# Kernel tuning notes

Hardware: AMD Instinct MI355X
Metric: run time of the kernel (lower is better)

## Reference

```python
import jax, jax.numpy as jnp
import numpy as np

N_HEAD = 16
MASK_PENALTY = 10000.0


def setup_inputs() -> dict:
    key = jax.random.key(0)
    k1, k2, k3 = jax.random.split(key, 3)
    B, S, D = 2, 2048, 1024
    x = jax.random.normal(k1, (B, S, D), dtype=jnp.float32)
    w_attn = jax.random.normal(k2, (D, 3 * D), dtype=jnp.float32) * 0.02
    b_attn = jnp.zeros((3 * D,), dtype=jnp.float32)
    w_proj = jax.random.normal(k3, (D, D), dtype=jnp.float32) * 0.02
    b_proj = jnp.zeros((D,), dtype=jnp.float32)
    return {"x": x, "w_attn": w_attn, "b_attn": b_attn, "w_proj": w_proj, "b_proj": b_proj}


def _split_heads(t, n_head):
    B, S, D = t.shape
    return t.reshape(B, S, n_head, D // n_head).transpose(0, 2, 1, 3)  # [B,H,S,dh]


def reference(x, w_attn, b_attn, w_proj, b_proj):
    B, S, D = x.shape
    qkv = x @ w_attn + b_attn  # fused QKV conv1d: [B,S,3D]
    q, k, v = jnp.split(qkv, 3, axis=2)
    q = _split_heads(q, N_HEAD)
    k = _split_heads(k, N_HEAD)
    v = _split_heads(v, N_HEAD)
    dh = D // N_HEAD
    w = jnp.einsum("bhqd,bhkd->bhqk", q, k) / jnp.sqrt(jnp.asarray(dh, dtype=q.dtype))
    # GPT-2 additive causal mask: w*b - 10000*(1-b)
    i = jnp.arange(S)[:, None]
    j = jnp.arange(S)[None, :]
    b = (i >= j).astype(w.dtype)  # nd == ns here
    w = w * b - MASK_PENALTY * (1.0 - b)
    w = jax.nn.softmax(w, axis=-1)
    a = jnp.einsum("bhqk,bhkd->bhqd", w, v)  # [B,H,S,dh]
    a = a.transpose(0, 2, 1, 3).reshape(B, S, D)  # merge heads
    return a @ w_proj + b_proj
```

## Files before the change

kernel.cpp:

```cpp
#include <hip/hip_runtime.h>
#include <hip/hip_bf16.h>


typedef short short8 __attribute__((ext_vector_type(8)));
typedef float f32x4 __attribute__((ext_vector_type(4)));

__device__ __forceinline__ unsigned short f2b(float f) {
    unsigned int x;
    __builtin_memcpy(&x, &f, 4);
    unsigned int r = x + 0x7FFF + ((x >> 16) & 1);
    return (unsigned short)(r >> 16);
}

__device__ __forceinline__ unsigned int pk2(float a, float b) {
    __hip_bfloat162 h = __float22bfloat162_rn(make_float2(a, b));
    unsigned int u;
    __builtin_memcpy(&u, &h, 4);
    return u;
}

__device__ __forceinline__ void load_lds16(const unsigned short* g, unsigned short* l) {
    __builtin_amdgcn_global_load_lds(
        (const __attribute__((address_space(1))) unsigned int*)g,
        (__attribute__((address_space(3))) unsigned int*)l, 16, 0, 0);
}

__global__ __launch_bounds__(256) void prep(const float* __restrict__ x, unsigned int* __restrict__ xb,
                                            const float* __restrict__ wA, unsigned short* __restrict__ wtA,
                                            const float* __restrict__ wP, unsigned short* __restrict__ wtP) {
    const int bx = blockIdx.x, tid = threadIdx.x;
    if (bx < 1024) {
#pragma unroll
        for (int j = 0; j < 4; j++) {
            int i = (bx * 1024 + j * 256 + tid) * 4;
            float4 f = *(const float4*)(x + i);
            uint2 p;
            p.x = pk2(f.x, f.y);
            p.y = pk2(f.z, f.w);
            *(uint2*)(xb + i / 2) = p;
        }
        return;
    }
    __shared__ unsigned short T[64][72];
    const float* in;
    unsigned short* out;
    int R, C, r0, c0;
    if (bx < 1792) { int t = bx - 1024; c0 = (t % 48) * 64; r0 = (t / 48) * 64; in = wA; out = wtA; R = 1024; C = 3072; }
    else           { int t = bx - 1792; c0 = (t % 16) * 64; r0 = (t / 16) * 64; in = wP; out = wtP; R = 1024; C = 1024; }
    const int ty = tid >> 4, tx = tid & 15;
#pragma unroll
    for (int i = 0; i < 4; i++) {
        int row = ty + i * 16;
        float4 f = *(const float4*)(in + (size_t)(r0 + row) * C + c0 + tx * 4);
        T[tx * 4 + 0][row] = f2b(f.x);
        T[tx * 4 + 1][row] = f2b(f.y);
        T[tx * 4 + 2][row] = f2b(f.z);
        T[tx * 4 + 3][row] = f2b(f.w);
    }
    __syncthreads();
    const int c = tid >> 2, rq = tid & 3;
    const uint4* s = (const uint4*)&T[c][rq * 16];
    uint4 a = s[0], b = s[1];
    unsigned short* dst = out + (size_t)(c0 + c) * R + r0 + rq * 16;
    *(uint4*)dst = a;
    *(uint4*)(dst + 8) = b;
}

__global__ __launch_bounds__(256) void qkv_gemm(const unsigned short* __restrict__ X,
                                                const unsigned short* __restrict__ WT,
                                                const float* __restrict__ bias,
                                                unsigned short* __restrict__ Qo,
                                                unsigned short* __restrict__ Ko,
                                                unsigned short* __restrict__ Vt) {
    __shared__ __align__(16) unsigned short SM[16384];
    unsigned short* As = SM;
    unsigned short* Bs = SM + 8192;
    const int tid = threadIdx.x;
    const int w = tid >> 6, l = tid & 63, l15 = l & 15, quad = l >> 4;
    const int wr = w >> 1, wc = w & 1;
    const int m0 = blockIdx.y * 128, n0 = blockIdx.x * 128;

    const int sr = w * 16 + (l >> 2);
    const int gch = (l & 3) ^ ((l >> 3) & 3);
    const unsigned short* Asrc = X + (size_t)(m0 + sr) * 1024 + gch * 8;
    const unsigned short* Bsrc = WT + (size_t)(n0 + sr) * 1024 + gch * 8;
    const int rswz = (l15 >> 1) & 3;

    f32x4 acc[4][4];
#pragma unroll
    for (int mt = 0; mt < 4; mt++)
#pragma unroll
        for (int nt = 0; nt < 4; nt++) acc[mt][nt] = (f32x4){0.f, 0.f, 0.f, 0.f};

    load_lds16(Asrc, &As[tid * 8]);
    load_lds16(Asrc + 65536, &As[2048 + tid * 8]);
    load_lds16(Bsrc, &Bs[tid * 8]);
    load_lds16(Bsrc + 65536, &Bs[2048 + tid * 8]);

    for (int k0 = 0; k0 < 1024; k0 += 32) {
        const int c = (k0 >> 5) & 1;
        __syncthreads();
        if (k0 + 32 < 1024) {
            const int pc = 1 - c;
            load_lds16(Asrc + k0 + 32, &As[pc * 4096 + tid * 8]);
            load_lds16(Asrc + 65536 + k0 + 32, &As[pc * 4096 + 2048 + tid * 8]);
            load_lds16(Bsrc + k0 + 32, &Bs[pc * 4096 + tid * 8]);
            load_lds16(Bsrc + 65536 + k0 + 32, &Bs[pc * 4096 + 2048 + tid * 8]);
        }

        short8 af[4], bfr[4];
#pragma unroll
        for (int mt = 0; mt < 4; mt++)
            af[mt] = *(const short8*)&As[c * 4096 + (wr * 64 + mt * 16 + l15) * 32 + ((quad ^ rswz) * 8)];
#pragma unroll
        for (int nt = 0; nt < 4; nt++)
            bfr[nt] = *(const short8*)&Bs[c * 4096 + (wc * 64 + nt * 16 + l15) * 32 + ((quad ^ rswz) * 8)];
#pragma unroll
        for (int mt = 0; mt < 4; mt++)
#pragma unroll
            for (int nt = 0; nt < 4; nt++)
                acc[mt][nt] = __builtin_amdgcn_mfma_f32_16x16x32_bf16(af[mt], bfr[nt], acc[mt][nt], 0, 0, 0);
    }

    const int which = n0 >> 10;
    const int c0 = n0 & 1023;
    float bv[4];
#pragma unroll
    for (int nt = 0; nt < 4; nt++) bv[nt] = bias[n0 + wc * 64 + nt * 16 + l15];

    if (which < 2) {
        const float scale = (which == 1) ? 0.125f : 1.0f;
        unsigned short* dst = (which == 0) ? Qo : Ko;
#pragma unroll
        for (int mt = 0; mt < 4; mt++)
#pragma unroll
            for (int nt = 0; nt < 4; nt++)
#pragma unroll
                for (int r = 0; r < 4; r++) {
                    int mg = m0 + wr * 64 + mt * 16 + quad * 4 + r;
                    int cg = c0 + wc * 64 + nt * 16 + l15;
                    float v = (acc[mt][nt][r] + bv[nt]) * scale;
                    int h = cg >> 6, d = cg & 63;
                    dst[(((size_t)(mg >> 11) * 16 + h) * 2048 + (mg & 2047)) * 64 + d] = f2b(v);
                }
    } else {
        const int b = m0 >> 11, sbase = m0 & 2047, h0 = c0 >> 6;
#pragma unroll
        for (int p = 0; p < 2; p++) {
            __syncthreads();
            if (wc == p) {
#pragma unroll
                for (int mt = 0; mt < 4; mt++)
#pragma unroll
                    for (int nt = 0; nt < 4; nt++)
#pragma unroll
                        for (int r = 0; r < 4; r++) {
                            float v = acc[mt][nt][r] + bv[nt];
                            int d = nt * 16 + l15;
                            int mloc = wr * 64 + mt * 16 + quad * 4 + r;
                            SM[d * 128 + (((mloc >> 4) ^ (d & 7)) << 4) + (mloc & 15)] = f2b(v);
                        }
            }
            __syncthreads();
            const int d = tid >> 2, q4 = tid & 3;
            size_t gb = ((size_t)((b * 16 + h0 + p) * 64 + d)) * 2048 + sbase + q4 * 32;
#pragma unroll
            for (int half = 0; half < 2; half++) {
                int mc = q4 * 2 + half;
                const uint4* s = (const uint4*)&SM[d * 128 + ((mc ^ (d & 7)) << 4)];
                *(uint4*)(Vt + gb + half * 16) = s[0];
                *(uint4*)(Vt + gb + half * 16 + 8) = s[1];
            }
        }
    }
}

__global__ __launch_bounds__(256) void attn_k(const unsigned short* __restrict__ Q,
                                              const unsigned short* __restrict__ K,
                                              const unsigned short* __restrict__ Vt,
                                              unsigned short* __restrict__ Om) {
    __shared__ __align__(16) unsigned short SM[20480];
    unsigned short* Ks0 = SM;
    unsigned short* Vts0 = SM + 8192;
    unsigned short* QP = SM + 16384;

    const int tid = threadIdx.x;
    const int w = tid >> 6, l = tid & 63, l15 = l & 15, quad = l >> 4;
    const int wq = w >> 1, ws = w & 1;
    const int bid = blockIdx.x;
    const int pi = bid >> 5;
    const int hb = bid & 31;
    const unsigned short* Qb = Q + (size_t)hb * 131072;
    const unsigned short* Kb = K + (size_t)hb * 131072;
    const unsigned short* Vb = Vt + (size_t)hb * 131072;

    const int sr = w * 8 + (l >> 3);
    const int gch = (l & 7) ^ (l >> 3);
    const int swz7 = l15 & 7;
    const int b = hb >> 4, h = hb & 15;

    short8 ones;
#pragma unroll
    for (int j = 0; j < 8; j++) ones[j] = (short)0x3F80;

    for (int half = 0; half < 2; half++) {
        const int qt = half ? pi : (31 - pi);
        const int q0 = qt * 64;

        if (half) __syncthreads();

        load_lds16(Qb + (q0 + sr) * 64 + gch * 8, &QP[tid * 8]);
        load_lds16(Qb + (q0 + 32 + sr) * 64 + gch * 8, &QP[2048 + tid * 8]);
        load_lds16(Kb + sr * 64 + gch * 8, &Ks0[tid * 8]);
        load_lds16(Kb + (32 + sr) * 64 + gch * 8, &Ks0[2048 + tid * 8]);
        load_lds16(Vb + sr * 2048 + gch * 8, &Vts0[tid * 8]);
        load_lds16(Vb + (32 + sr) * 2048 + gch * 8, &Vts0[2048 + tid * 8]);
        __syncthreads();

        short8 qf[2][2];
#pragma unroll
        for (int qnt = 0; qnt < 2; qnt++)
#pragma unroll
            for (int ks = 0; ks < 2; ks++)
                qf[qnt][ks] = *(const short8*)&QP[(wq * 32 + qnt * 16 + l15) * 64 + (((ks * 4 + quad) ^ swz7) << 3)];

        f32x4 o[2][4], lacc[2];
#pragma unroll
        for (int pmt = 0; pmt < 2; pmt++) {
            lacc[pmt] = (f32x4){0.f, 0.f, 0.f, 0.f};
#pragma unroll
            for (int dnt = 0; dnt < 4; dnt++) o[pmt][dnt] = (f32x4){0.f, 0.f, 0.f, 0.f};
        }

        for (int kt = 0; kt <= qt; kt++) {
            const int c = kt & 1;
            const unsigned short* Ksc = Ks0 + c * 4096;
            const unsigned short* Vtsc = Vts0 + c * 4096;
            __syncthreads();
            if (kt < qt) {
                const int kn = (kt + 1) * 64, pc = 1 - c;
                load_lds16(Kb + (kn + sr) * 64 + gch * 8, &Ks0[pc * 4096 + tid * 8]);
                load_lds16(Kb + (kn + 32 + sr) * 64 + gch * 8, &Ks0[pc * 4096 + 2048 + tid * 8]);
                load_lds16(Vb + sr * 2048 + kn + gch * 8, &Vts0[pc * 4096 + tid * 8]);
                load_lds16(Vb + (32 + sr) * 2048 + kn + gch * 8, &Vts0[pc * 4096 + 2048 + tid * 8]);
            }

            f32x4 sa[2][2];
#pragma unroll
            for (int smt = 0; smt < 2; smt++)
#pragma unroll
                for (int qnt = 0; qnt < 2; qnt++) sa[smt][qnt] = (f32x4){0.f, 0.f, 0.f, 0.f};
#pragma unroll
            for (int ks = 0; ks < 2; ks++) {
                short8 kf[2];
#pragma unroll
                for (int smt = 0; smt < 2; smt++)
                    kf[smt] = *(const short8*)&Ksc[(ws * 32 + smt * 16 + l15) * 64 + (((ks * 4 + quad) ^ swz7) << 3)];
#pragma unroll
                for (int smt = 0; smt < 2; smt++)
#pragma unroll
                    for (int qnt = 0; qnt < 2; qnt++)
                        sa[smt][qnt] = __builtin_amdgcn_mfma_f32_16x16x32_bf16(kf[smt], qf[qnt][ks], sa[smt][qnt], 0, 0, 0);
            }

            float pv[2][2][4];
            if (kt == qt) {
#pragma unroll
                for (int smt = 0; smt < 2; smt++)
#pragma unroll
                    for (int qnt = 0; qnt < 2; qnt++)
#pragma unroll
                        for (int r = 0; r < 4; r++) {
                            int cg = kt * 64 + ws * 32 + smt * 16 + quad * 4 + r;
                            int rg = q0 + wq * 32 + qnt * 16 + l15;
                            pv[smt][qnt][r] = (cg <= rg) ? __expf(sa[smt][qnt][r]) : 0.f;
                        }
            } else {
#pragma unroll
                for (int smt = 0; smt < 2; smt++)
#pragma unroll
                    for (int qnt = 0; qnt < 2; qnt++)
#pragma unroll
                        for (int r = 0; r < 4; r++)
                            pv[smt][qnt][r] = __expf(sa[smt][qnt][r]);
            }

#pragma unroll
            for (int smt = 0; smt < 2; smt++)
#pragma unroll
                for (int qnt = 0; qnt < 2; qnt++) {
                    int q = wq * 32 + qnt * 16 + l15;
                    int sb = ws * 32 + smt * 16 + quad * 4;
                    int ch = (sb >> 3) ^ (q & 7);
                    int a16 = q * 64 + (ch << 3) + (sb & 7);
                    uint2 u;
                    u.x = pk2(pv[smt][qnt][0], pv[smt][qnt][1]);
                    u.y = pk2(pv[smt][qnt][2], pv[smt][qnt][3]);
                    *(uint2*)&QP[a16] = u;
                }
            asm volatile("s_waitcnt lgkmcnt(0)" ::: "memory");

            short8 pf[2];
#pragma unroll
            for (int pmt = 0; pmt < 2; pmt++) {
                pf[pmt] = *(const short8*)&QP[(wq * 32 + pmt * 16 + l15) * 64 + (((ws * 4 + quad) ^ swz7) << 3)];
                lacc[pmt] = __builtin_amdgcn_mfma_f32_16x16x32_bf16(pf[pmt], ones, lacc[pmt], 0, 0, 0);
            }
#pragma unroll
            for (int dnt = 0; dnt < 4; dnt++) {
                short8 vf = *(const short8*)&Vtsc[(dnt * 16 + l15) * 64 + (((ws * 4 + quad) ^ swz7) << 3)];
#pragma unroll
                for (int pmt = 0; pmt < 2; pmt++)
                    o[pmt][dnt] = __builtin_amdgcn_mfma_f32_16x16x32_bf16(pf[pmt], vf, o[pmt][dnt], 0, 0, 0);
            }
        }

        __syncthreads();
        float* red = (float*)SM;
        float* myp = red + (wq * 64 + l) * 41;
        if (ws == 1) {
#pragma unroll
            for (int pmt = 0; pmt < 2; pmt++) {
#pragma unroll
                for (int dnt = 0; dnt < 4; dnt++)
#pragma unroll
                    for (int r = 0; r < 4; r++) myp[pmt * 16 + dnt * 4 + r] = o[pmt][dnt][r];
#pragma unroll
                for (int r = 0; r < 4; r++) myp[32 + pmt * 4 + r] = lacc[pmt][r];
            }
        }
        __syncthreads();
        if (ws == 0) {
            float inv[2][4];
#pragma unroll
            for (int pmt = 0; pmt < 2; pmt++)
#pragma unroll
                for (int r = 0; r < 4; r++)
                    inv[pmt][r] = 1.0f / (lacc[pmt][r] + myp[32 + pmt * 4 + r]);
#pragma unroll
            for (int pmt = 0; pmt < 2; pmt++)
#pragma unroll
                for (int dnt = 0; dnt < 4; dnt++)
#pragma unroll
                    for (int r = 0; r < 4; r++) {
                        float val = (o[pmt][dnt][r] + myp[pmt * 16 + dnt * 4 + r]) * inv[pmt][r];
                        int sg = q0 + wq * 32 + pmt * 16 + quad * 4 + r;
                        int col = h * 64 + dnt * 16 + l15;
                        Om[((size_t)(b * 2048 + sg)) * 1024 + col] = f2b(val);
                    }
        }
    }
}

__global__ __launch_bounds__(256) void proj_gemm(const unsigned short* __restrict__ A,
                                                 const unsigned short* __restrict__ WT,
                                                 const float* __restrict__ bias,
                                                 float* __restrict__ out) {
    __shared__ __align__(16) unsigned short As[2][4096];
    __shared__ __align__(16) unsigned short Bs[2][2048];
    const int tid = threadIdx.x;
    const int w = tid >> 6, l = tid & 63, l15 = l & 15, quad = l >> 4;
    const int wr = w >> 1, wc = w & 1;
    const int m0 = blockIdx.y * 128, n0 = blockIdx.x * 64;

    const int sr = w * 16 + (l >> 2);
    const int gch = (l & 3) ^ ((l >> 3) & 3);
    const unsigned short* Asrc = A + (size_t)(m0 + sr) * 1024 + gch * 8;
    const unsigned short* Bsrc = WT + (size_t)(n0 + sr) * 1024 + gch * 8;
    const int rswz = (l15 >> 1) & 3;

    f32x4 acc[4][2];
#pragma unroll
    for (int mt = 0; mt < 4; mt++)
#pragma unroll
        for (int nt = 0; nt < 2; nt++) acc[mt][nt] = (f32x4){0.f, 0.f, 0.f, 0.f};

    load_lds16(Asrc, &As[0][tid * 8]);
    load_lds16(Asrc + 65536, &As[0][2048 + tid * 8]);
    load_lds16(Bsrc, &Bs[0][tid * 8]);

    for (int k0 = 0; k0 < 1024; k0 += 32) {
        const int c = (k0 >> 5) & 1;
        __syncthreads();
        if (k0 + 32 < 1024) {
            const int pc = 1 - c;
            load_lds16(Asrc + k0 + 32, &As[pc][tid * 8]);
            load_lds16(Asrc + 65536 + k0 + 32, &As[pc][2048 + tid * 8]);
            load_lds16(Bsrc + k0 + 32, &Bs[pc][tid * 8]);
        }

        short8 af[4], bfr[2];
#pragma unroll
        for (int mt = 0; mt < 4; mt++)
            af[mt] = *(const short8*)&As[c][(wr * 64 + mt * 16 + l15) * 32 + ((quad ^ rswz) * 8)];
#pragma unroll
        for (int nt = 0; nt < 2; nt++)
            bfr[nt] = *(const short8*)&Bs[c][(wc * 32 + nt * 16 + l15) * 32 + ((quad ^ rswz) * 8)];
#pragma unroll
        for (int mt = 0; mt < 4; mt++)
#pragma unroll
            for (int nt = 0; nt < 2; nt++)
                acc[mt][nt] = __builtin_amdgcn_mfma_f32_16x16x32_bf16(af[mt], bfr[nt], acc[mt][nt], 0, 0, 0);
    }

#pragma unroll
    for (int mt = 0; mt < 4; mt++)
#pragma unroll
        for (int nt = 0; nt < 2; nt++)
#pragma unroll
            for (int r = 0; r < 4; r++) {
                int mg = m0 + wr * 64 + mt * 16 + quad * 4 + r;
                int ng = n0 + wc * 32 + nt * 16 + l15;
                out[(size_t)mg * 1024 + ng] = acc[mt][nt][r] + bias[ng];
            }
}

extern "C" void kernel_launch(void* const* d_in, const int* in_sizes, int n_in,
                              void* d_out, int out_size, void* d_ws, size_t ws_size,
                              hipStream_t stream) {
    (void)in_sizes; (void)n_in; (void)out_size; (void)ws_size;
    const float* x      = (const float*)d_in[0];
    const float* w_attn = (const float*)d_in[1];
    const float* b_attn = (const float*)d_in[2];
    const float* w_proj = (const float*)d_in[3];
    const float* b_proj = (const float*)d_in[4];
    float* out = (float*)d_out;
    unsigned short* ws = (unsigned short*)d_ws;

    unsigned short* wtA  = ws;
    unsigned short* wtP  = wtA + 3145728;
    unsigned short* Qw   = wtP + 1048576;
    unsigned short* Kw   = Qw + 4194304;
    unsigned short* Vtw  = Kw + 4194304;
    unsigned short* XbOm = Vtw + 4194304;

    prep<<<2048, 256, 0, stream>>>(x, (unsigned int*)XbOm, w_attn, wtA, w_proj, wtP);
    qkv_gemm<<<dim3(24, 32), 256, 0, stream>>>(XbOm, wtA, b_attn, Qw, Kw, Vtw);
    attn_k<<<512, 256, 0, stream>>>(Qw, Kw, Vtw, XbOm);
    proj_gemm<<<dim3(16, 32), 256, 0, stream>>>(XbOm, wtP, b_proj, out);
}
```

Baseline: 176.5 us.

## Triple-buffer LDS pipelines with one barrier per step; split attention blocks per query tile

In all three GEMM-like kernels, the double-buffered LDS loop with a full __syncthreads becomes a three-stage ring. Each step issues the next tile's global-to-LDS loads, then runs s_waitcnt vmcnt(N) plus s_barrier, so only the older tile must land and one load group stays in flight. The attention kernel no longer pairs a long and a short causal query tile per block; it launches 1024 blocks with one query tile each and relies on the scheduler to balance the uneven work. LDS use per block grows, which may lower occupancy, and the last iterations issue redundant dummy loads.

```diff
diff --git a/kernel.cpp b/kernel.cpp
--- a/kernel.cpp
+++ b/kernel.cpp
@@ -4,6 +4,10 @@
 
 typedef short short8 __attribute__((ext_vector_type(8)));
 typedef float f32x4 __attribute__((ext_vector_type(4)));
+
+#define WAITB4 asm volatile("s_waitcnt vmcnt(4)\n\ts_barrier" ::: "memory")
+#define WAITB3 asm volatile("s_waitcnt vmcnt(3)\n\ts_barrier" ::: "memory")
+#define DRAIN0 asm volatile("s_waitcnt vmcnt(0)" ::: "memory")
 
 __device__ __forceinline__ unsigned short f2b(float f) {
     unsigned int x;
@@ -72,9 +76,9 @@
                                                 unsigned short* __restrict__ Qo,
                                                 unsigned short* __restrict__ Ko,
                                                 unsigned short* __restrict__ Vt) {
-    __shared__ __align__(16) unsigned short SM[16384];
+    __shared__ __align__(16) unsigned short SM[24576];
     unsigned short* As = SM;
-    unsigned short* Bs = SM + 8192;
+    unsigned short* Bs = SM + 12288;
     const int tid = threadIdx.x;
     const int w = tid >> 6, l = tid & 63, l15 = l & 15, quad = l >> 4;
     const int wr = w >> 1, wc = w & 1;
@@ -97,16 +101,15 @@
     load_lds16(Bsrc, &Bs[tid * 8]);
     load_lds16(Bsrc + 65536, &Bs[2048 + tid * 8]);
 
-    for (int k0 = 0; k0 < 1024; k0 += 32) {
-        const int c = (k0 >> 5) & 1;
-        __syncthreads();
-        if (k0 + 32 < 1024) {
-            const int pc = 1 - c;
-            load_lds16(Asrc + k0 + 32, &As[pc * 4096 + tid * 8]);
-            load_lds16(Asrc + 65536 + k0 + 32, &As[pc * 4096 + 2048 + tid * 8]);
-            load_lds16(Bsrc + k0 + 32, &Bs[pc * 4096 + tid * 8]);
-            load_lds16(Bsrc + 65536 + k0 + 32, &Bs[pc * 4096 + 2048 + tid * 8]);
-        }
+    for (int i = 0; i < 32; i++) {
+        const int k0 = i * 32;
+        const int c = i % 3, pb = (i + 1) % 3;
+        const int kn = (k0 + 32 < 1024) ? k0 + 32 : 0;
+        load_lds16(Asrc + kn, &As[pb * 4096 + tid * 8]);
+        load_lds16(Asrc + 65536 + kn, &As[pb * 4096 + 2048 + tid * 8]);
+        load_lds16(Bsrc + kn, &Bs[pb * 4096 + tid * 8]);
+        load_lds16(Bsrc + 65536 + kn, &Bs[pb * 4096 + 2048 + tid * 8]);
+        WAITB4;
 
         short8 af[4], bfr[4];
 #pragma unroll
@@ -121,6 +124,7 @@
             for (int nt = 0; nt < 4; nt++)
                 acc[mt][nt] = __builtin_amdgcn_mfma_f32_16x16x32_bf16(af[mt], bfr[nt], acc[mt][nt], 0, 0, 0);
     }
+    DRAIN0;
 
     const int which = n0 >> 10;
     const int c0 = n0 & 1023;
@@ -179,17 +183,18 @@
                                               const unsigned short* __restrict__ K,
                                               const unsigned short* __restrict__ Vt,
                                               unsigned short* __restrict__ Om) {
-    __shared__ __align__(16) unsigned short SM[20480];
+    __shared__ __align__(16) unsigned short SM[28672];
     unsigned short* Ks0 = SM;
-    unsigned short* Vts0 = SM + 8192;
-    unsigned short* QP = SM + 16384;
+    unsigned short* Vts0 = SM + 12288;
+    unsigned short* QP = SM + 24576;
 
     const int tid = threadIdx.x;
     const int w = tid >> 6, l = tid & 63, l15 = l & 15, quad = l >> 4;
     const int wq = w >> 1, ws = w & 1;
     const int bid = blockIdx.x;
-    const int pi = bid >> 5;
+    const int qt = 31 - (bid >> 5);
     const int hb = bid & 31;
+    const int q0 = qt * 64;
     const unsigned short* Qb = Q + (size_t)hb * 131072;
     const unsigned short* Kb = K + (size_t)hb * 131072;
     const unsigned short* Vb = Vt + (size_t)hb * 131072;
@@ -197,158 +202,149 @@
     const int sr = w * 8 + (l >> 3);
     const int gch = (l & 7) ^ (l >> 3);
     const int swz7 = l15 & 7;
-    const int b = hb >> 4, h = hb & 15;
+
+    load_lds16(Qb + (q0 + sr) * 64 + gch * 8, &QP[tid * 8]);
+    load_lds16(Qb + (q0 + 32 + sr) * 64 + gch * 8, &QP[2048 + tid * 8]);
+    load_lds16(Kb + sr * 64 + gch * 8, &Ks0[tid * 8]);
+    load_lds16(Kb + (32 + sr) * 64 + gch * 8, &Ks0[2048 + tid * 8]);
+    load_lds16(Vb + sr * 2048 + gch * 8, &Vts0[tid * 8]);
+    load_lds16(Vb + (32 + sr) * 2048 + gch * 8, &Vts0[2048 + tid * 8]);
+    __syncthreads();
+
+    short8 qf[2][2];
+#pragma unroll
+    for (int qnt = 0; qnt < 2; qnt++)
+#pragma unroll
+        for (int ks = 0; ks < 2; ks++)
+            qf[qnt][ks] = *(const short8*)&QP[(wq * 32 + qnt * 16 + l15) * 64 + (((ks * 4 + quad) ^ swz7) << 3)];
 
     short8 ones;
 #pragma unroll
     for (int j = 0; j < 8; j++) ones[j] = (short)0x3F80;
 
-    for (int half = 0; half < 2; half++) {
-        const int qt = half ? pi : (31 - pi);
-        const int q0 = qt * 64;
-
-        if (half) __syncthreads();
-
-        load_lds16(Qb + (q0 + sr) * 64 + gch * 8, &QP[tid * 8]);
-        load_lds16(Qb + (q0 + 32 + sr) * 64 + gch * 8, &QP[2048 + tid * 8]);
-        load_lds16(Kb + sr * 64 + gch * 8, &Ks0[tid * 8]);
-        load_lds16(Kb + (32 + sr) * 64 + gch * 8, &Ks0[2048 + tid * 8]);
-        load_lds16(Vb + sr * 2048 + gch * 8, &Vts0[tid * 8]);
-        load_lds16(Vb + (32 + sr) * 2048 + gch * 8, &Vts0[2048 + tid * 8]);
-        __syncthreads();
-
-        short8 qf[2][2];
-#pragma unroll
-        for (int qnt = 0; qnt < 2; qnt++)
-#pragma unroll
-            for (int ks = 0; ks < 2; ks++)
-                qf[qnt][ks] = *(const short8*)&QP[(wq * 32 + qnt * 16 + l15) * 64 + (((ks * 4 + quad) ^ swz7) << 3)];
-
-        f32x4 o[2][4], lacc[2];
+    f32x4 o[2][4], lacc[2];
+#pragma unroll
+    for (int pmt = 0; pmt < 2; pmt++) {
+        lacc[pmt] = (f32x4){0.f, 0.f, 0.f, 0.f};
+#pragma unroll
+        for (int dnt = 0; dnt < 4; dnt++) o[pmt][dnt] = (f32x4){0.f, 0.f, 0.f, 0.f};
+    }
+
+    for (int kt = 0; kt <= qt; kt++) {
+        const int c = kt % 3, pb = (kt + 1) % 3;
+        const unsigned short* Ksc = Ks0 + c * 4096;
+        const unsigned short* Vtsc = Vts0 + c * 4096;
+        const int kn = ((kt < qt) ? (kt + 1) : kt) * 64;
+        load_lds16(Kb + (kn + sr) * 64 + gch * 8, &Ks0[pb * 4096 + tid * 8]);
+        load_lds16(Kb + (kn + 32 + sr) * 64 + gch * 8, &Ks0[pb * 4096 + 2048 + tid * 8]);
+        load_lds16(Vb + sr * 2048 + kn + gch * 8, &Vts0[pb * 4096 + tid * 8]);
+        load_lds16(Vb + (32 + sr) * 2048 + kn + gch * 8, &Vts0[pb * 4096 + 2048 + tid * 8]);
+        WAITB4;
+
+        f32x4 sa[2][2];
+#pragma unroll
+        for (int smt = 0; smt < 2; smt++)
+#pragma unroll
+            for (int qnt = 0; qnt < 2; qnt++) sa[smt][qnt] = (f32x4){0.f, 0.f, 0.f, 0.f};
+#pragma unroll
+        for (int ks = 0; ks < 2; ks++) {
+            short8 kf[2];
+#pragma unroll
+            for (int smt = 0; smt < 2; smt++)
+                kf[smt] = *(const short8*)&Ksc[(ws * 32 + smt * 16 + l15) * 64 + (((ks * 4 + quad) ^ swz7) << 3)];
+#pragma unroll
+            for (int smt = 0; smt < 2; smt++)
+#pragma unroll
+                for (int qnt = 0; qnt < 2; qnt++)
+                    sa[smt][qnt] = __builtin_amdgcn_mfma_f32_16x16x32_bf16(kf[smt], qf[qnt][ks], sa[smt][qnt], 0, 0, 0);
+        }
+
+        float pv[2][2][4];
+        if (kt == qt) {
+#pragma unroll
+            for (int smt = 0; smt < 2; smt++)
+#pragma unroll
+                for (int qnt = 0; qnt < 2; qnt++)
+#pragma unroll
+                    for (int r = 0; r < 4; r++) {
+                        int cg = kt * 64 + ws * 32 + smt * 16 + quad * 4 + r;
+                        int rg = q0 + wq * 32 + qnt * 16 + l15;
+                        pv[smt][qnt][r] = (cg <= rg) ? __expf(sa[smt][qnt][r]) : 0.f;
+                    }
+        } else {
+#pragma unroll
+            for (int smt = 0; smt < 2; smt++)
+#pragma unroll
+                for (int qnt = 0; qnt < 2; qnt++)
+#pragma unroll
+                    for (int r = 0; r < 4; r++)
+                        pv[smt][qnt][r] = __expf(sa[smt][qnt][r]);
+        }
+
+#pragma unroll
+        for (int smt = 0; smt < 2; smt++)
+#pragma unroll
+            for (int qnt = 0; qnt < 2; qnt++) {
+                int q = wq * 32 + qnt * 16 + l15;
+                int sb = ws * 32 + smt * 16 + quad * 4;
+                int ch = (sb >> 3) ^ (q & 7);
+                int a16 = q * 64 + (ch << 3) + (sb & 7);
+                uint2 u;
+                u.x = pk2(pv[smt][qnt][0], pv[smt][qnt][1]);
+                u.y = pk2(pv[smt][qnt][2], pv[smt][qnt][3]);
+                *(uint2*)&QP[a16] = u;
+            }
+        asm volatile("s_waitcnt lgkmcnt(0)" ::: "memory");
+
+        short8 pf[2];
 #pragma unroll
         for (int pmt = 0; pmt < 2; pmt++) {
-            lacc[pmt] = (f32x4){0.f, 0.f, 0.f, 0.f};
-#pragma unroll
-            for (int dnt = 0; dnt < 4; dnt++) o[pmt][dnt] = (f32x4){0.f, 0.f, 0.f, 0.f};
-        }
-
-        for (int kt = 0; kt <= qt; kt++) {
-            const int c = kt & 1;
-            const unsigned short* Ksc = Ks0 + c * 4096;
-            const unsigned short* Vtsc = Vts0 + c * 4096;
-            __syncthreads();
-            if (kt < qt) {
-                const int kn = (kt + 1) * 64, pc = 1 - c;
-                load_lds16(Kb + (kn + sr) * 64 + gch * 8, &Ks0[pc * 4096 + tid * 8]);
-                load_lds16(Kb + (kn + 32 + sr) * 64 + gch * 8, &Ks0[pc * 4096 + 2048 + tid * 8]);
-                load_lds16(Vb + sr * 2048 + kn + gch * 8, &Vts0[pc * 4096 + tid * 8]);
-                load_lds16(Vb + (32 + sr) * 2048 + kn + gch * 8, &Vts0[pc * 4096 + 2048 + tid * 8]);
-            }
-
-            f32x4 sa[2][2];
-#pragma unroll
-            for (int smt = 0; smt < 2; smt++)
-#pragma unroll
-                for (int qnt = 0; qnt < 2; qnt++) sa[smt][qnt] = (f32x4){0.f, 0.f, 0.f, 0.f};
-#pragma unroll
-            for (int ks = 0; ks < 2; ks++) {
-                short8 kf[2];
-#pragma unroll
-                for (int smt = 0; smt < 2; smt++)
-                    kf[smt] = *(const short8*)&Ksc[(ws * 32 + smt * 16 + l15) * 64 + (((ks * 4 + quad) ^ swz7) << 3)];
-#pragma unroll
-                for (int smt = 0; smt < 2; smt++)
-#pragma unroll
-                    for (int qnt = 0; qnt < 2; qnt++)
-                        sa[smt][qnt] = __builtin_amdgcn_mfma_f32_16x16x32_bf16(kf[smt], qf[qnt][ks], sa[smt][qnt], 0, 0, 0);
-            }
-
-            float pv[2][2][4];
-            if (kt == qt) {
-#pragma unroll
-                for (int smt = 0; smt < 2; smt++)
-#pragma unroll
-                    for (int qnt = 0; qnt < 2; qnt++)
-#pragma unroll
-                        for (int r = 0; r < 4; r++) {
-                            int cg = kt * 64 + ws * 32 + smt * 16 + quad * 4 + r;
-                            int rg = q0 + wq * 32 + qnt * 16 + l15;
-                            pv[smt][qnt][r] = (cg <= rg) ? __expf(sa[smt][qnt][r]) : 0.f;
-                        }
-            } else {
-#pragma unroll
-                for (int smt = 0; smt < 2; smt++)
-#pragma unroll
-                    for (int qnt = 0; qnt < 2; qnt++)
-#pragma unroll
-                        for (int r = 0; r < 4; r++)
-                            pv[smt][qnt][r] = __expf(sa[smt][qnt][r]);
-            }
-
-#pragma unroll
-            for (int smt = 0; smt < 2; smt++)
-#pragma unroll
-                for (int qnt = 0; qnt < 2; qnt++) {
-                    int q = wq * 32 + qnt * 16 + l15;
-                    int sb = ws * 32 + smt * 16 + quad * 4;
-                    int ch = (sb >> 3) ^ (q & 7);
-                    int a16 = q * 64 + (ch << 3) + (sb & 7);
-                    uint2 u;
-                    u.x = pk2(pv[smt][qnt][0], pv[smt][qnt][1]);
-                    u.y = pk2(pv[smt][qnt][2], pv[smt][qnt][3]);
-                    *(uint2*)&QP[a16] = u;
+            pf[pmt] = *(const short8*)&QP[(wq * 32 + pmt * 16 + l15) * 64 + (((ws * 4 + quad) ^ swz7) << 3)];
+            lacc[pmt] = __builtin_amdgcn_mfma_f32_16x16x32_bf16(pf[pmt], ones, lacc[pmt], 0, 0, 0);
+        }
+#pragma unroll
+        for (int dnt = 0; dnt < 4; dnt++) {
+            short8 vf = *(const short8*)&Vtsc[(dnt * 16 + l15) * 64 + (((ws * 4 + quad) ^ swz7) << 3)];
+#pragma unroll
+            for (int pmt = 0; pmt < 2; pmt++)
+                o[pmt][dnt] = __builtin_amdgcn_mfma_f32_16x16x32_bf16(pf[pmt], vf, o[pmt][dnt], 0, 0, 0);
+        }
+    }
+
+    __syncthreads();
+    float* red = (float*)SM;
+    float* myp = red + (wq * 64 + l) * 41;
+    if (ws == 1) {
+#pragma unroll
+        for (int pmt = 0; pmt < 2; pmt++) {
+#pragma unroll
+            for (int dnt = 0; dnt < 4; dnt++)
+#pragma unroll
+                for (int r = 0; r < 4; r++) myp[pmt * 16 + dnt * 4 + r] = o[pmt][dnt][r];
+#pragma unroll
+            for (int r = 0; r < 4; r++) myp[32 + pmt * 4 + r] = lacc[pmt][r];
+        }
+    }
+    __syncthreads();
+    if (ws == 0) {
+        const int b = hb >> 4, h = hb & 15;
+        float inv[2][4];
+#pragma unroll
+        for (int pmt = 0; pmt < 2; pmt++)
+#pragma unroll
+            for (int r = 0; r < 4; r++)
+                inv[pmt][r] = 1.0f / (lacc[pmt][r] + myp[32 + pmt * 4 + r]);
+#pragma unroll
+        for (int pmt = 0; pmt < 2; pmt++)
+#pragma unroll
+            for (int dnt = 0; dnt < 4; dnt++)
+#pragma unroll
+                for (int r = 0; r < 4; r++) {
+                    float val = (o[pmt][dnt][r] + myp[pmt * 16 + dnt * 4 + r]) * inv[pmt][r];
+                    int sg = q0 + wq * 32 + pmt * 16 + quad * 4 + r;
+                    int col = h * 64 + dnt * 16 + l15;
+                    Om[((size_t)(b * 2048 + sg)) * 1024 + col] = f2b(val);
                 }
-            asm volatile("s_waitcnt lgkmcnt(0)" ::: "memory");
-
-            short8 pf[2];
-#pragma unroll
-            for (int pmt = 0; pmt < 2; pmt++) {
-                pf[pmt] = *(const short8*)&QP[(wq * 32 + pmt * 16 + l15) * 64 + (((ws * 4 + quad) ^ swz7) << 3)];
-                lacc[pmt] = __builtin_amdgcn_mfma_f32_16x16x32_bf16(pf[pmt], ones, lacc[pmt], 0, 0, 0);
-            }
-#pragma unroll
-            for (int dnt = 0; dnt < 4; dnt++) {
-                short8 vf = *(const short8*)&Vtsc[(dnt * 16 + l15) * 64 + (((ws * 4 + quad) ^ swz7) << 3)];
-#pragma unroll
-                for (int pmt = 0; pmt < 2; pmt++)
-                    o[pmt][dnt] = __builtin_amdgcn_mfma_f32_16x16x32_bf16(pf[pmt], vf, o[pmt][dnt], 0, 0, 0);
-            }
-        }
-
-        __syncthreads();
-        float* red = (float*)SM;
-        float* myp = red + (wq * 64 + l) * 41;
-        if (ws == 1) {
-#pragma unroll
-            for (int pmt = 0; pmt < 2; pmt++) {
-#pragma unroll
-                for (int dnt = 0; dnt < 4; dnt++)
-#pragma unroll
-                    for (int r = 0; r < 4; r++) myp[pmt * 16 + dnt * 4 + r] = o[pmt][dnt][r];
-#pragma unroll
-                for (int r = 0; r < 4; r++) myp[32 + pmt * 4 + r] = lacc[pmt][r];
-            }
-        }
-        __syncthreads();
-        if (ws == 0) {
-            float inv[2][4];
-#pragma unroll
-            for (int pmt = 0; pmt < 2; pmt++)
-#pragma unroll
-                for (int r = 0; r < 4; r++)
-                    inv[pmt][r] = 1.0f / (lacc[pmt][r] + myp[32 + pmt * 4 + r]);
-#pragma unroll
-            for (int pmt = 0; pmt < 2; pmt++)
-#pragma unroll
-                for (int dnt = 0; dnt < 4; dnt++)
-#pragma unroll
-                    for (int r = 0; r < 4; r++) {
-                        float val = (o[pmt][dnt][r] + myp[pmt * 16 + dnt * 4 + r]) * inv[pmt][r];
-                        int sg = q0 + wq * 32 + pmt * 16 + quad * 4 + r;
-                        int col = h * 64 + dnt * 16 + l15;
-                        Om[((size_t)(b * 2048 + sg)) * 1024 + col] = f2b(val);
-                    }
-        }
     }
 }
 
@@ -356,8 +352,9 @@
                                                  const unsigned short* __restrict__ WT,
                                                  const float* __restrict__ bias,
                                                  float* __restrict__ out) {
-    __shared__ __align__(16) unsigned short As[2][4096];
-    __shared__ __align__(16) unsigned short Bs[2][2048];
+    __shared__ __align__(16) unsigned short SM[18432];
+    unsigned short* As = SM;
+    unsigned short* Bs = SM + 12288;
     const int tid = threadIdx.x;
     const int w = tid >> 6, l = tid & 63, l15 = l & 15, quad = l >> 4;
     const int wr = w >> 1, wc = w & 1;
@@ -375,33 +372,33 @@
 #pragma unroll
         for (int nt = 0; nt < 2; nt++) acc[mt][nt] = (f32x4){0.f, 0.f, 0.f, 0.f};
 
-    load_lds16(Asrc, &As[0][tid * 8]);
-    load_lds16(Asrc + 65536, &As[0][2048 + tid * 8]);
-    load_lds16(Bsrc, &Bs[0][tid * 8]);
-
-    for (int k0 = 0; k0 < 1024; k0 += 32) {
-        const int c = (k0 >> 5) & 1;
-        __syncthreads();
-        if (k0 + 32 < 1024) {
-            const int pc = 1 - c;
-            load_lds16(Asrc + k0 + 32, &As[pc][tid * 8]);
-            load_lds16(Asrc + 65536 + k0 + 32, &As[pc][2048 + tid * 8]);
-            load_lds16(Bsrc + k0 + 32, &Bs[pc][tid * 8]);
-        }
+    load_lds16(Asrc, &As[tid * 8]);
+    load_lds16(Asrc + 65536, &As[2048 + tid * 8]);
+    load_lds16(Bsrc, &Bs[tid * 8]);
+
+    for (int i = 0; i < 32; i++) {
+        const int k0 = i * 32;
+        const int c = i % 3, pb = (i + 1) % 3;
+        const int kn = (k0 + 32 < 1024) ? k0 + 32 : 0;
+        load_lds16(Asrc + kn, &As[pb * 4096 + tid * 8]);
+        load_lds16(Asrc + 65536 + kn, &As[pb * 4096 + 2048 + tid * 8]);
+        load_lds16(Bsrc + kn, &Bs[pb * 2048 + tid * 8]);
+        WAITB3;
 
         short8 af[4], bfr[2];
 #pragma unroll
         for (int mt = 0; mt < 4; mt++)
-            af[mt] = *(const short8*)&As[c][(wr * 64 + mt * 16 + l15) * 32 + ((quad ^ rswz) * 8)];
+            af[mt] = *(const short8*)&As[c * 4096 + (wr * 64 + mt * 16 + l15) * 32 + ((quad ^ rswz) * 8)];
 #pragma unroll
         for (int nt = 0; nt < 2; nt++)
-            bfr[nt] = *(const short8*)&Bs[c][(wc * 32 + nt * 16 + l15) * 32 + ((quad ^ rswz) * 8)];
+            bfr[nt] = *(const short8*)&Bs[c * 2048 + (wc * 32 + nt * 16 + l15) * 32 + ((quad ^ rswz) * 8)];
 #pragma unroll
         for (int mt = 0; mt < 4; mt++)
 #pragma unroll
             for (int nt = 0; nt < 2; nt++)
                 acc[mt][nt] = __builtin_amdgcn_mfma_f32_16x16x32_bf16(af[mt], bfr[nt], acc[mt][nt], 0, 0, 0);
     }
+    DRAIN0;
 
 #pragma unroll
     for (int mt = 0; mt < 4; mt++)
@@ -436,6 +433,6 @@
 
     prep<<<2048, 256, 0, stream>>>(x, (unsigned int*)XbOm, w_attn, wtA, w_proj, wtP);
     qkv_gemm<<<dim3(24, 32), 256, 0, stream>>>(XbOm, wtA, b_attn, Qw, Kw, Vtw);
-    attn_k<<<512, 256, 0, stream>>>(Qw, Kw, Vtw, XbOm);
+    attn_k<<<1024, 256, 0, stream>>>(Qw, Kw, Vtw, XbOm);
     proj_gemm<<<dim3(16, 32), 256, 0, stream>>>(XbOm, wtP, b_proj, out);
 }
```

New measurement: 182.5 us. 1.03x slower.
